# Optimization experiments

Hardware: AMD Instinct MI355X
Metric: run time of the kernel (lower is better)

Reference implementation:

```python
import jax, jax.numpy as jnp
import numpy as np

B, S, D, H = 2, 2048, 1024, 16
HD = D // H  # head_dim = 64

def setup_inputs() -> dict:
    key = jax.random.key(0)
    ks = jax.random.split(key, 5)
    scale = 1.0 / np.sqrt(D)
    x = jax.random.normal(ks[0], (B, S, D), dtype=jnp.float32)
    Wq = jax.random.normal(ks[1], (D, D), dtype=jnp.float32) * scale
    Wk = jax.random.normal(ks[2], (D, D), dtype=jnp.float32) * scale
    Wv = jax.random.normal(ks[3], (D, D), dtype=jnp.float32) * scale
    Wf = jax.random.normal(ks[4], (D, D), dtype=jnp.float32) * scale
    z = jnp.zeros((D,), dtype=jnp.float32)
    return {"x": x, "Wq": Wq, "bq": z, "Wk": Wk, "bk": z, "Wv": Wv, "bv": z, "Wf": Wf, "bf": z}

def reference(x, Wq, bq, Wk, bk, Wv, bv, Wf, bf):
    # Linear layers follow torch convention: y = x @ W.T + b
    def split_heads(t):  # [B,S,D] -> [B,H,S,HD]
        return t.reshape(B, S, H, HD).transpose(0, 2, 1, 3)
    q = split_heads(x @ Wq.T + bq)
    k = split_heads(x @ Wk.T + bk)
    v = split_heads(x @ Wv.T + bv)
    scores = jnp.einsum('bhqd,bhkd->bhqk', q, k) / jnp.sqrt(jnp.float32(HD))
    causal = jnp.tril(jnp.ones((S, S), dtype=bool))  # [S,S]
    scores = jnp.where(causal[None, None], scores, -jnp.inf)
    attn = jax.nn.softmax(scores, axis=-1)
    out = jnp.einsum('bhqk,bhkd->bhqd', attn, v)
    out = out.transpose(0, 2, 1, 3).reshape(B, S, D)
    return out @ Wf.T + bf
```

## Files before the change

kernel.cpp:

```cpp
#include <hip/hip_runtime.h>
#include <stdint.h>

#define B_  2
#define S_  2048
#define D_  1024
#define H_  16
#define HD_ 64
#define M_  (B_*S_)

typedef __bf16 bf16x8 __attribute__((ext_vector_type(8)));
typedef float  f32x4  __attribute__((ext_vector_type(4)));

typedef const __attribute__((address_space(1))) void* gas_ptr;
typedef __attribute__((address_space(3))) void* las_ptr;

__device__ __forceinline__ uint16_t f32_to_bf16(float f) {
  uint32_t u = __float_as_uint(f);
  u += 0x7FFFu + ((u >> 16) & 1u);
  return (uint16_t)(u >> 16);
}

__device__ __forceinline__ uint16_t f32_to_bf16_rtz(float f) {
  return (uint16_t)(__float_as_uint(f) >> 16);
}

__device__ __forceinline__ void g2l16(const uint16_t* g, uint16_t* l) {
  __builtin_amdgcn_global_load_lds((gas_ptr)g, (las_ptr)l, 16, 0, 0);
}

__device__ __forceinline__ int swz_src(int s) {
  return (s >> 2) * D_ + (((s & 3) ^ ((s >> 3) & 3)) * 8);
}

__global__ void cast_all(const float* __restrict__ x,
                         const float* __restrict__ wq, const float* __restrict__ wk,
                         const float* __restrict__ wv, const float* __restrict__ wf,
                         uint16_t* __restrict__ xb,
                         uint16_t* __restrict__ wqb, uint16_t* __restrict__ wkb,
                         uint16_t* __restrict__ wvb, uint16_t* __restrict__ wfb) {
  const int X4 = M_ * D_ / 4;
  const int W4 = D_ * D_ / 4;
  int i = blockIdx.x * 256 + threadIdx.x;
  const float* src; uint16_t* dst; int off;
  if (i < X4) { src = x; dst = xb; off = i; }
  else {
    int j = i - X4;
    int w = j >> 18;
    off = j & (W4 - 1);
    src = (w == 0) ? wq : (w == 1) ? wk : (w == 2) ? wv : wf;
    dst = (w == 0) ? wqb : (w == 1) ? wkb : (w == 2) ? wvb : wfb;
  }
  float4 v = ((const float4*)src)[off];
  ushort4 o;
  o.x = f32_to_bf16(v.x); o.y = f32_to_bf16(v.y);
  o.z = f32_to_bf16(v.z); o.w = f32_to_bf16(v.w);
  ((ushort4*)dst)[off] = o;
}

__device__ __forceinline__ void gemm_tile_128_bk64(
    const uint16_t* __restrict__ A, const uint16_t* __restrict__ B,
    int am0, int bn0, uint16_t* As, uint16_t* Bs, f32x4 (&acc)[4][4])
{
  const int tid  = threadIdx.x;
  const int wave = tid >> 6;
  const int lane = tid & 63;
  const int quad = lane >> 4;
  const int l16  = lane & 15;
  const int wm = (wave >> 1) * 64;
  const int wn = (wave & 1) * 64;
  const int sw = quad ^ ((l16 >> 1) & 3);

  #pragma unroll
  for (int i = 0; i < 4; ++i)
    #pragma unroll
    for (int j = 0; j < 4; ++j)
      #pragma unroll
      for (int e = 0; e < 4; ++e)
        acc[i][j][e] = 0.f;

  const int s0 = wave * 64 + lane;
  const int s1 = s0 + 256;
  const int so0 = swz_src(s0), so1 = swz_src(s1);
  uint16_t* lA0 = As + (size_t)(wave * 64) * 8;
  uint16_t* lA1 = As + (size_t)(256 + wave * 64) * 8;
  uint16_t* lB0 = Bs + (size_t)(wave * 64) * 8;
  uint16_t* lB1 = Bs + (size_t)(256 + wave * 64) * 8;
  const uint16_t* gA0 = A + (size_t)am0 * D_ + so0;
  const uint16_t* gA1 = A + (size_t)am0 * D_ + so1;
  const uint16_t* gB0 = B + (size_t)bn0 * D_ + so0;
  const uint16_t* gB1 = B + (size_t)bn0 * D_ + so1;

  for (int k0 = 0; k0 < D_; k0 += 64) {
    g2l16(gA0 + k0,      lA0);
    g2l16(gA1 + k0,      lA1);
    g2l16(gB0 + k0,      lB0);
    g2l16(gB1 + k0,      lB1);
    g2l16(gA0 + k0 + 32, lA0 + 4096);
    g2l16(gA1 + k0 + 32, lA1 + 4096);
    g2l16(gB0 + k0 + 32, lB0 + 4096);
    g2l16(gB1 + k0 + 32, lB1 + 4096);
    __syncthreads();
    bf16x8 af0[4], af1[4], bf0[4], bf1[4];
    #pragma unroll
    for (int mt = 0; mt < 4; ++mt) {
      const int ro = ((wm + mt * 16 + l16) * 4 + sw) * 8;
      af0[mt] = *(const bf16x8*)(As + ro);
      af1[mt] = *(const bf16x8*)(As + 4096 + ro);
    }
    #pragma unroll
    for (int nt = 0; nt < 4; ++nt) {
      const int ro = ((wn + nt * 16 + l16) * 4 + sw) * 8;
      bf0[nt] = *(const bf16x8*)(Bs + ro);
      bf1[nt] = *(const bf16x8*)(Bs + 4096 + ro);
    }
    #pragma unroll
    for (int mt = 0; mt < 4; ++mt)
      #pragma unroll
      for (int nt = 0; nt < 4; ++nt) {
        acc[mt][nt] = __builtin_amdgcn_mfma_f32_16x16x32_bf16(
            af0[mt], bf0[nt], acc[mt][nt], 0, 0, 0);
        acc[mt][nt] = __builtin_amdgcn_mfma_f32_16x16x32_bf16(
            af1[mt], bf1[nt], acc[mt][nt], 0, 0, 0);
      }
    __syncthreads();
  }
}

__global__ __launch_bounds__(256)
void qkv_gemm(const uint16_t* __restrict__ xb,
              const uint16_t* __restrict__ wqb, const uint16_t* __restrict__ wkb,
              const uint16_t* __restrict__ wvb,
              const float* __restrict__ bqv, const float* __restrict__ bkv,
              const float* __restrict__ bvv,
              uint16_t* __restrict__ qout, uint16_t* __restrict__ kout,
              uint16_t* __restrict__ vtout)
{
  __shared__ __align__(16) uint16_t As[2 * 128 * 32];
  __shared__ __align__(16) uint16_t Bs[2 * 128 * 32];
  const int wsel = blockIdx.x >> 3;
  const int nsel = blockIdx.x & 7;
  const int mtile = blockIdx.y;
  const int lane = threadIdx.x & 63, wave = threadIdx.x >> 6;
  const int quad = lane >> 4, l16 = lane & 15;
  const int wm = (wave >> 1) * 64, wn = (wave & 1) * 64;

  const uint16_t *Ap, *Bp;
  int m0e, n0e;
  if (wsel < 2) {
    Ap = xb; Bp = (wsel == 0) ? wqb : wkb;
    m0e = mtile * 128; n0e = nsel * 128;
  } else {
    Ap = wvb; Bp = xb;
    m0e = nsel * 128; n0e = mtile * 128;
  }
  f32x4 acc[4][4];
  gemm_tile_128_bk64(Ap, Bp, m0e, n0e, As, Bs, acc);

  if (wsel < 2) {
    const float* bias = (wsel == 0) ? bqv : bkv;
    uint16_t* outp = (wsel == 0) ? qout : kout;
    const float scl = (wsel == 0) ? 0.18033688f : 1.0f;
    #pragma unroll
    for (int nt = 0; nt < 4; ++nt) {
      const int n = n0e + wn + nt * 16 + l16;
      const int h = n >> 6, hd = n & 63;
      const float bia = bias[n];
      #pragma unroll
      for (int mt = 0; mt < 4; ++mt) {
        #pragma unroll
        for (int r = 0; r < 4; ++r) {
          const int m = m0e + wm + mt * 16 + quad * 4 + r;
          const int bb = m >> 11, s = m & (S_ - 1);
          outp[(((size_t)(bb * H_ + h)) * S_ + s) * HD_ + hd] =
              f32_to_bf16((acc[mt][nt][r] + bia) * scl);
        }
      }
    }
  } else {
    #pragma unroll
    for (int mt = 0; mt < 4; ++mt) {
      #pragma unroll
      for (int r = 0; r < 4; ++r) {
        const int m = m0e + wm + mt * 16 + quad * 4 + r;
        const int h = m >> 6, hd = m & 63;
        const float bia = bvv[m];
        #pragma unroll
        for (int nt = 0; nt < 4; ++nt) {
          const int n = n0e + wn + nt * 16 + l16;
          const int bb = n >> 11, s = n & (S_ - 1);
          vtout[(((size_t)(bb * H_ + h)) * HD_ + hd) * S_ + s] =
              f32_to_bf16(acc[mt][nt][r] + bia);
        }
      }
    }
  }
}

__global__ __launch_bounds__(256)
void flash_attn(const uint16_t* __restrict__ qb, const uint16_t* __restrict__ kb,
                const uint16_t* __restrict__ vtb, uint16_t* __restrict__ ao)
{
  __shared__ __align__(16) uint16_t ks[2][64 * 32];
  __shared__ __align__(16) uint16_t vs[2][64 * 32];
  __shared__ __align__(16) uint16_t p_lds[4][16][72];

  const int bh = blockIdx.x;
  const int qt = (int)(gridDim.y - 1u - blockIdx.y);
  const int wave = threadIdx.x >> 6, lane = threadIdx.x & 63;
  const int quad = lane >> 4, l16 = lane & 15;
  const int sw = quad ^ ((l16 >> 1) & 3);
  const int q0 = qt * 64;

  const uint16_t* Q  = qb  + (size_t)bh * S_ * HD_;
  const uint16_t* Kp = kb  + (size_t)bh * S_ * HD_;
  const uint16_t* Vt = vtb + (size_t)bh * HD_ * S_;

  const int qrow = q0 + wave * 16;
  bf16x8 aq0 = *(const bf16x8*)(Q + (size_t)(qrow + l16) * HD_ + quad * 8);
  bf16x8 aq1 = *(const bf16x8*)(Q + (size_t)(qrow + l16) * HD_ + 32 + quad * 8);

  const int srow = lane >> 2;
  const int schk = (lane & 3) ^ ((lane >> 3) & 3);
  const uint16_t* sb[4]; uint16_t* sdst[4]; int sstep[4];
  #pragma unroll
  for (int j = 0; j < 4; ++j) {
    const int g = wave * 4 + j;
    if (g < 8) {
      const int c = (g >> 2) & 1, rb = g & 3;
      sdst[j] = &ks[c][rb * 512];
      sb[j] = Kp + (size_t)(rb * 16 + srow) * HD_ + c * 32 + schk * 8;
      sstep[j] = 64 * HD_;
    } else {
      const int gg = g - 8, c = (gg >> 2) & 1, rb = gg & 3;
      sdst[j] = &vs[c][rb * 512];
      sb[j] = Vt + (size_t)(rb * 16 + srow) * S_ + c * 32 + schk * 8;
      sstep[j] = 64;
    }
  }

  float lpart[4];
  f32x4 o[4];
  #pragma unroll
  for (int r = 0; r < 4; ++r) lpart[r] = 0.f;
  #pragma unroll
  for (int t = 0; t < 4; ++t)
    #pragma unroll
    for (int e = 0; e < 4; ++e) o[t][e] = 0.f;

  const int rowid = qrow + quad * 4;

  for (int kt = 0; kt <= qt; ++kt) {
    const int kbase = kt * 64;
    const bool diag = (kt == qt);

    #pragma unroll
    for (int j = 0; j < 4; ++j) {
      g2l16(sb[j], sdst[j]);
      sb[j] += sstep[j];
    }
    __syncthreads();

    bf16x8 kf0[4], kf1[4];
    #pragma unroll
    for (int nt = 0; nt < 4; ++nt) {
      kf0[nt] = *(const bf16x8*)(&ks[0][((nt * 16 + l16) * 4 + sw) * 8]);
      kf1[nt] = *(const bf16x8*)(&ks[1][((nt * 16 + l16) * 4 + sw) * 8]);
    }
    f32x4 sacc[4];
    #pragma unroll
    for (int nt = 0; nt < 4; ++nt) {
      #pragma unroll
      for (int e = 0; e < 4; ++e) sacc[nt][e] = 0.f;
      sacc[nt] = __builtin_amdgcn_mfma_f32_16x16x32_bf16(aq0, kf0[nt], sacc[nt], 0, 0, 0);
      sacc[nt] = __builtin_amdgcn_mfma_f32_16x16x32_bf16(aq1, kf1[nt], sacc[nt], 0, 0, 0);
    }

    bf16x8 vf0[4], vf1[4];
    #pragma unroll
    for (int t = 0; t < 4; ++t) {
      vf0[t] = *(const bf16x8*)(&vs[0][((t * 16 + l16) * 4 + sw) * 8]);
      vf1[t] = *(const bf16x8*)(&vs[1][((t * 16 + l16) * 4 + sw) * 8]);
    }

    #pragma unroll
    for (int nt = 0; nt < 4; ++nt) {
      const int kkc = kbase + nt * 16 + l16;
      #pragma unroll
      for (int r = 0; r < 4; ++r) {
        float p = __builtin_amdgcn_exp2f(sacc[nt][r]);
        if (diag && (kkc > rowid + r)) p = 0.f;
        lpart[r] += p;
        p_lds[wave][quad * 4 + r][nt * 16 + l16] = f32_to_bf16_rtz(p);
      }
    }

    bf16x8 ap0 = *(const bf16x8*)(&p_lds[wave][l16][quad * 8]);
    bf16x8 ap1 = *(const bf16x8*)(&p_lds[wave][l16][32 + quad * 8]);
    #pragma unroll
    for (int t = 0; t < 4; ++t) {
      o[t] = __builtin_amdgcn_mfma_f32_16x16x32_bf16(ap0, vf0[t], o[t], 0, 0, 0);
      o[t] = __builtin_amdgcn_mfma_f32_16x16x32_bf16(ap1, vf1[t], o[t], 0, 0, 0);
    }
    __syncthreads();
  }

  #pragma unroll
  for (int r = 0; r < 4; ++r) {
    lpart[r] += __shfl_xor(lpart[r], 1, 64);
    lpart[r] += __shfl_xor(lpart[r], 2, 64);
    lpart[r] += __shfl_xor(lpart[r], 4, 64);
    lpart[r] += __shfl_xor(lpart[r], 8, 64);
  }
  const int bb = bh >> 4, h = bh & 15;
  #pragma unroll
  for (int t = 0; t < 4; ++t) {
    #pragma unroll
    for (int r = 0; r < 4; ++r) {
      const float ov = o[t][r] / lpart[r];
      ao[((size_t)(bb * S_ + rowid + r)) * D_ + h * HD_ + t * 16 + l16] =
          f32_to_bf16(ov);
    }
  }
}

__global__ __launch_bounds__(256)
void out_gemm(const uint16_t* __restrict__ ab, const uint16_t* __restrict__ wfb,
              const float* __restrict__ bfv, float* __restrict__ out)
{
  __shared__ __align__(16) uint16_t As[2 * 64 * 32];
  __shared__ __align__(16) uint16_t Bs[2 * 128 * 32];
  const int m0 = blockIdx.y * 64;
  const int n0 = blockIdx.x * 128;
  const int lane = threadIdx.x & 63, wave = threadIdx.x >> 6;
  const int quad = lane >> 4, l16 = lane & 15;
  const int wm = (wave >> 1) * 32, wn = (wave & 1) * 64;
  const int sw = quad ^ ((l16 >> 1) & 3);

  f32x4 acc[2][4];
  #pragma unroll
  for (int i = 0; i < 2; ++i)
    #pragma unroll
    for (int j = 0; j < 4; ++j)
      #pragma unroll
      for (int e = 0; e < 4; ++e)
        acc[i][j][e] = 0.f;

  const int sA  = wave * 64 + lane;
  const int sB1 = sA + 256;
  const int soA = swz_src(sA), soB1 = swz_src(sB1);
  uint16_t* lA  = As + (size_t)(wave * 64) * 8;
  uint16_t* lB0 = Bs + (size_t)(wave * 64) * 8;
  uint16_t* lB1 = Bs + (size_t)(256 + wave * 64) * 8;
  const uint16_t* gA  = ab  + (size_t)m0 * D_ + soA;
  const uint16_t* gB0 = wfb + (size_t)n0 * D_ + soA;
  const uint16_t* gB1 = wfb + (size_t)n0 * D_ + soB1;

  for (int k0 = 0; k0 < D_; k0 += 64) {
    g2l16(gA  + k0,      lA);
    g2l16(gB0 + k0,      lB0);
    g2l16(gB1 + k0,      lB1);
    g2l16(gA  + k0 + 32, lA  + 2048);
    g2l16(gB0 + k0 + 32, lB0 + 4096);
    g2l16(gB1 + k0 + 32, lB1 + 4096);
    __syncthreads();
    bf16x8 af0[2], af1[2], bf0[4], bf1[4];
    #pragma unroll
    for (int mt = 0; mt < 2; ++mt) {
      const int ro = ((wm + mt * 16 + l16) * 4 + sw) * 8;
      af0[mt] = *(const bf16x8*)(As + ro);
      af1[mt] = *(const bf16x8*)(As + 2048 + ro);
    }
    #pragma unroll
    for (int nt = 0; nt < 4; ++nt) {
      const int ro = ((wn + nt * 16 + l16) * 4 + sw) * 8;
      bf0[nt] = *(const bf16x8*)(Bs + ro);
      bf1[nt] = *(const bf16x8*)(Bs + 4096 + ro);
    }
    #pragma unroll
    for (int mt = 0; mt < 2; ++mt)
      #pragma unroll
      for (int nt = 0; nt < 4; ++nt) {
        acc[mt][nt] = __builtin_amdgcn_mfma_f32_16x16x32_bf16(
            af0[mt], bf0[nt], acc[mt][nt], 0, 0, 0);
        acc[mt][nt] = __builtin_amdgcn_mfma_f32_16x16x32_bf16(
            af1[mt], bf1[nt], acc[mt][nt], 0, 0, 0);
      }
    __syncthreads();
  }

  #pragma unroll
  for (int nt = 0; nt < 4; ++nt) {
    const int n = n0 + wn + nt * 16 + l16;
    const float bia = bfv[n];
    #pragma unroll
    for (int mt = 0; mt < 2; ++mt) {
      #pragma unroll
      for (int r = 0; r < 4; ++r) {
        const int m = m0 + wm + mt * 16 + quad * 4 + r;
        out[(size_t)m * D_ + n] = acc[mt][nt][r] + bia;
      }
    }
  }
}

extern "C" void kernel_launch(void* const* d_in, const int* in_sizes, int n_in,
                              void* d_out, int out_size, void* d_ws, size_t ws_size,
                              hipStream_t stream) {
  (void)in_sizes; (void)n_in; (void)out_size; (void)ws_size;
  const float* x  = (const float*)d_in[0];
  const float* Wq = (const float*)d_in[1];
  const float* bq = (const float*)d_in[2];
  const float* Wk = (const float*)d_in[3];
  const float* bk = (const float*)d_in[4];
  const float* Wv = (const float*)d_in[5];
  const float* bv = (const float*)d_in[6];
  const float* Wf = (const float*)d_in[7];
  const float* bf = (const float*)d_in[8];
  float* out = (float*)d_out;

  uint16_t* ws = (uint16_t*)d_ws;
  uint16_t* xb   = ws;
  uint16_t* wqb  = xb  + (size_t)M_ * D_;
  uint16_t* wkb  = wqb + (size_t)D_ * D_;
  uint16_t* wvb  = wkb + (size_t)D_ * D_;
  uint16_t* wfb  = wvb + (size_t)D_ * D_;
  uint16_t* qbuf = wfb + (size_t)D_ * D_;
  uint16_t* kbuf = qbuf + (size_t)M_ * D_;
  uint16_t* vtb  = kbuf + (size_t)M_ * D_;
  uint16_t* aob  = vtb  + (size_t)M_ * D_;

  const int CAST_BLOCKS = (M_ * D_ / 4 + 4 * (D_ * D_ / 4)) / 256;
  cast_all<<<CAST_BLOCKS, 256, 0, stream>>>(x, Wq, Wk, Wv, Wf,
                                            xb, wqb, wkb, wvb, wfb);

  qkv_gemm<<<dim3(24, 32), 256, 0, stream>>>(xb, wqb, wkb, wvb, bq, bk, bv,
                                             qbuf, kbuf, vtb);
  flash_attn<<<dim3(32, 32), 256, 0, stream>>>(qbuf, kbuf, vtb, aob);
  out_gemm<<<dim3(8, 64), 256, 0, stream>>>(aob, wfb, bf, out);
}
```

Before: 182.1 us.

## Enlarge QKV GEMM tile to 256x256 with double-buffered LDS prefetch

The QKV projection GEMM now uses 512-thread blocks computing 256x256 output tiles instead of 128x128, with each wave covering 128x64. LDS is double-buffered so the next K-slice is loaded asynchronously while MFMAs run on the current one, using explicit barriers, waitcnts and priority bumps around the MFMA groups. The goal is more data reuse per LDS load and hiding global-load latency. The cost is higher register and LDS use, 128 KB of LDS per block, and a grid of only 192 blocks, which may underfill the GPU's compute units.

```diff
diff --git a/kernel.cpp b/kernel.cpp
--- a/kernel.cpp
+++ b/kernel.cpp
@@ -57,76 +57,7 @@
   ((ushort4*)dst)[off] = o;
 }
 
-__device__ __forceinline__ void gemm_tile_128_bk64(
-    const uint16_t* __restrict__ A, const uint16_t* __restrict__ B,
-    int am0, int bn0, uint16_t* As, uint16_t* Bs, f32x4 (&acc)[4][4])
-{
-  const int tid  = threadIdx.x;
-  const int wave = tid >> 6;
-  const int lane = tid & 63;
-  const int quad = lane >> 4;
-  const int l16  = lane & 15;
-  const int wm = (wave >> 1) * 64;
-  const int wn = (wave & 1) * 64;
-  const int sw = quad ^ ((l16 >> 1) & 3);
-
-  #pragma unroll
-  for (int i = 0; i < 4; ++i)
-    #pragma unroll
-    for (int j = 0; j < 4; ++j)
-      #pragma unroll
-      for (int e = 0; e < 4; ++e)
-        acc[i][j][e] = 0.f;
-
-  const int s0 = wave * 64 + lane;
-  const int s1 = s0 + 256;
-  const int so0 = swz_src(s0), so1 = swz_src(s1);
-  uint16_t* lA0 = As + (size_t)(wave * 64) * 8;
-  uint16_t* lA1 = As + (size_t)(256 + wave * 64) * 8;
-  uint16_t* lB0 = Bs + (size_t)(wave * 64) * 8;
-  uint16_t* lB1 = Bs + (size_t)(256 + wave * 64) * 8;
-  const uint16_t* gA0 = A + (size_t)am0 * D_ + so0;
-  const uint16_t* gA1 = A + (size_t)am0 * D_ + so1;
-  const uint16_t* gB0 = B + (size_t)bn0 * D_ + so0;
-  const uint16_t* gB1 = B + (size_t)bn0 * D_ + so1;
-
-  for (int k0 = 0; k0 < D_; k0 += 64) {
-    g2l16(gA0 + k0,      lA0);
-    g2l16(gA1 + k0,      lA1);
-    g2l16(gB0 + k0,      lB0);
-    g2l16(gB1 + k0,      lB1);
-    g2l16(gA0 + k0 + 32, lA0 + 4096);
-    g2l16(gA1 + k0 + 32, lA1 + 4096);
-    g2l16(gB0 + k0 + 32, lB0 + 4096);
-    g2l16(gB1 + k0 + 32, lB1 + 4096);
-    __syncthreads();
-    bf16x8 af0[4], af1[4], bf0[4], bf1[4];
-    #pragma unroll
-    for (int mt = 0; mt < 4; ++mt) {
-      const int ro = ((wm + mt * 16 + l16) * 4 + sw) * 8;
-      af0[mt] = *(const bf16x8*)(As + ro);
-      af1[mt] = *(const bf16x8*)(As + 4096 + ro);
-    }
-    #pragma unroll
-    for (int nt = 0; nt < 4; ++nt) {
-      const int ro = ((wn + nt * 16 + l16) * 4 + sw) * 8;
-      bf0[nt] = *(const bf16x8*)(Bs + ro);
-      bf1[nt] = *(const bf16x8*)(Bs + 4096 + ro);
-    }
-    #pragma unroll
-    for (int mt = 0; mt < 4; ++mt)
-      #pragma unroll
-      for (int nt = 0; nt < 4; ++nt) {
-        acc[mt][nt] = __builtin_amdgcn_mfma_f32_16x16x32_bf16(
-            af0[mt], bf0[nt], acc[mt][nt], 0, 0, 0);
-        acc[mt][nt] = __builtin_amdgcn_mfma_f32_16x16x32_bf16(
-            af1[mt], bf1[nt], acc[mt][nt], 0, 0, 0);
-      }
-    __syncthreads();
-  }
-}
-
-__global__ __launch_bounds__(256)
+__global__ __launch_bounds__(512, 2)
 void qkv_gemm(const uint16_t* __restrict__ xb,
               const uint16_t* __restrict__ wqb, const uint16_t* __restrict__ wkb,
               const uint16_t* __restrict__ wvb,
@@ -135,26 +66,108 @@
               uint16_t* __restrict__ qout, uint16_t* __restrict__ kout,
               uint16_t* __restrict__ vtout)
 {
-  __shared__ __align__(16) uint16_t As[2 * 128 * 32];
-  __shared__ __align__(16) uint16_t Bs[2 * 128 * 32];
-  const int wsel = blockIdx.x >> 3;
-  const int nsel = blockIdx.x & 7;
+  __shared__ __align__(16) uint16_t As[2][2][8192];
+  __shared__ __align__(16) uint16_t Bs[2][2][8192];
+
+  const int wsel = blockIdx.x >> 2;
+  const int nsel = blockIdx.x & 3;
   const int mtile = blockIdx.y;
-  const int lane = threadIdx.x & 63, wave = threadIdx.x >> 6;
+  const int tid  = threadIdx.x;
+  const int lane = tid & 63, wave = tid >> 6;
   const int quad = lane >> 4, l16 = lane & 15;
-  const int wm = (wave >> 1) * 64, wn = (wave & 1) * 64;
+  const int wm = (wave >> 2) * 128;
+  const int wn = (wave & 3) * 64;
+  const int sw = quad ^ ((l16 >> 1) & 3);
 
   const uint16_t *Ap, *Bp;
   int m0e, n0e;
   if (wsel < 2) {
     Ap = xb; Bp = (wsel == 0) ? wqb : wkb;
-    m0e = mtile * 128; n0e = nsel * 128;
+    m0e = mtile * 256; n0e = nsel * 256;
   } else {
     Ap = wvb; Bp = xb;
-    m0e = nsel * 128; n0e = mtile * 128;
-  }
-  f32x4 acc[4][4];
-  gemm_tile_128_bk64(Ap, Bp, m0e, n0e, As, Bs, acc);
+    m0e = nsel * 256; n0e = mtile * 256;
+  }
+
+  const int so0 = swz_src(tid);
+  const int so1 = swz_src(tid + 512);
+  const uint16_t* gA = Ap + (size_t)m0e * D_;
+  const uint16_t* gB = Bp + (size_t)n0e * D_;
+  const int d0 = (wave * 64) * 8;
+  const int d1 = (512 + wave * 64) * 8;
+
+  f32x4 acc[8][4];
+  #pragma unroll
+  for (int i = 0; i < 8; ++i)
+    #pragma unroll
+    for (int j = 0; j < 4; ++j)
+      #pragma unroll
+      for (int e = 0; e < 4; ++e)
+        acc[i][j][e] = 0.f;
+
+  g2l16(gA + so0,      &As[0][0][d0]);
+  g2l16(gA + 32 + so0, &As[0][1][d0]);
+  g2l16(gB + so0,      &Bs[0][0][d0]);
+  g2l16(gB + 32 + so0, &Bs[0][1][d0]);
+  g2l16(gA + so1,      &As[0][0][d1]);
+  g2l16(gA + 32 + so1, &As[0][1][d1]);
+  g2l16(gB + so1,      &Bs[0][0][d1]);
+  g2l16(gB + 32 + so1, &Bs[0][1][d1]);
+  __syncthreads();
+
+  bf16x8 bfr[4][2], afr[2][2];
+  for (int t = 0; t < 16; ++t) {
+    const int c = t & 1, cn = c ^ 1;
+    const bool pf = (t < 15);
+    const int kn = (t + 1) * 64;
+
+    #pragma unroll
+    for (int nt = 0; nt < 4; ++nt) {
+      const int ro = ((wn + nt * 16 + l16) * 4 + sw) * 8;
+      bfr[nt][0] = *(const bf16x8*)(&Bs[c][0][ro]);
+      bfr[nt][1] = *(const bf16x8*)(&Bs[c][1][ro]);
+    }
+
+    #pragma unroll
+    for (int p = 0; p < 4; ++p) {
+      #pragma unroll
+      for (int i = 0; i < 2; ++i) {
+        const int ro = ((wm + (2 * p + i) * 16 + l16) * 4 + sw) * 8;
+        afr[i][0] = *(const bf16x8*)(&As[c][0][ro]);
+        afr[i][1] = *(const bf16x8*)(&As[c][1][ro]);
+      }
+      if (p == 0 && pf) {
+        g2l16(gA + kn + so0,      &As[cn][0][d0]);
+        g2l16(gA + kn + 32 + so0, &As[cn][1][d0]);
+        g2l16(gB + kn + so0,      &Bs[cn][0][d0]);
+        g2l16(gB + kn + 32 + so0, &Bs[cn][1][d0]);
+      }
+      if (p == 1 && pf) {
+        g2l16(gA + kn + so1,      &As[cn][0][d1]);
+        g2l16(gA + kn + 32 + so1, &As[cn][1][d1]);
+        g2l16(gB + kn + so1,      &Bs[cn][0][d1]);
+        g2l16(gB + kn + 32 + so1, &Bs[cn][1][d1]);
+      }
+      __builtin_amdgcn_s_barrier();
+      asm volatile("s_waitcnt lgkmcnt(0)" ::: "memory");
+      __builtin_amdgcn_sched_barrier(0);
+      __builtin_amdgcn_s_setprio(1);
+      #pragma unroll
+      for (int i = 0; i < 2; ++i)
+        #pragma unroll
+        for (int nt = 0; nt < 4; ++nt) {
+          acc[2 * p + i][nt] = __builtin_amdgcn_mfma_f32_16x16x32_bf16(
+              afr[i][0], bfr[nt][0], acc[2 * p + i][nt], 0, 0, 0);
+          acc[2 * p + i][nt] = __builtin_amdgcn_mfma_f32_16x16x32_bf16(
+              afr[i][1], bfr[nt][1], acc[2 * p + i][nt], 0, 0, 0);
+        }
+      __builtin_amdgcn_s_setprio(0);
+      if (p == 3) {
+        asm volatile("s_waitcnt vmcnt(0)" ::: "memory");
+      }
+      __builtin_amdgcn_s_barrier();
+    }
+  }
 
   if (wsel < 2) {
     const float* bias = (wsel == 0) ? bqv : bkv;
@@ -166,7 +179,7 @@
       const int h = n >> 6, hd = n & 63;
       const float bia = bias[n];
       #pragma unroll
-      for (int mt = 0; mt < 4; ++mt) {
+      for (int mt = 0; mt < 8; ++mt) {
         #pragma unroll
         for (int r = 0; r < 4; ++r) {
           const int m = m0e + wm + mt * 16 + quad * 4 + r;
@@ -178,7 +191,7 @@
     }
   } else {
     #pragma unroll
-    for (int mt = 0; mt < 4; ++mt) {
+    for (int mt = 0; mt < 8; ++mt) {
       #pragma unroll
       for (int r = 0; r < 4; ++r) {
         const int m = m0e + wm + mt * 16 + quad * 4 + r;
@@ -433,7 +446,7 @@
   cast_all<<<CAST_BLOCKS, 256, 0, stream>>>(x, Wq, Wk, Wv, Wf,
                                             xb, wqb, wkb, wvb, wfb);
 
-  qkv_gemm<<<dim3(24, 32), 256, 0, stream>>>(xb, wqb, wkb, wvb, bq, bk, bv,
+  qkv_gemm<<<dim3(12, 16), 512, 0, stream>>>(xb, wqb, wkb, wvb, bq, bk, bv,
                                              qbuf, kbuf, vtb);
   flash_attn<<<dim3(32, 32), 256, 0, stream>>>(qbuf, kbuf, vtb, aob);
   out_gemm<<<dim3(8, 64), 256, 0, stream>>>(aob, wfb, bf, out);
```

Measured after the change: 181.4 us. No clear change (-0.4%).
